# Kernel optimization log

Measured on AMD Instinct MI355X. Metric: run time of the kernel, lower is better.

Reference implementation:

```python
import jax, jax.numpy as jnp
import numpy as np

NUM_HEADS = 4
HEAD_K = 256
HEAD_V = 512
CHUNK = 64
GATE_NORMALIZER = 16.0
EPS = 1e-5


def _gla_chunk(q, k, v, gk):
    """Chunked gated linear attention.
    q,k,gk: [B,H,S,Dk]; v: [B,H,S,Dv]. gk is log-decay (<=0).
    Recurrence: S_t = diag(exp(gk_t)) S_{t-1} + k_t v_t^T ; o_t = scale * q_t S_t.
    """
    B, H, S, Dk = q.shape
    Dv = v.shape[-1]
    N = S // CHUNK
    scale = Dk ** -0.5

    def to_chunks(x):
        # [B,H,S,D] -> [N,B,H,C,D]
        return x.reshape(B, H, N, CHUNK, x.shape[-1]).transpose(2, 0, 1, 3, 4)

    qc, kc, vc, gkc = map(to_chunks, (q, k, v, gk))
    gc = jnp.cumsum(gkc, axis=-2)  # inclusive cumulative log-decay within chunk

    tri = jnp.tril(jnp.ones((CHUNK, CHUNK), dtype=q.dtype))  # causal incl. diagonal

    def step(Sstate, xs):
        qi, ki, vi, gi = xs  # [B,H,C,Dk]/[B,H,C,Dv]
        q_g = qi * jnp.exp(gi) * scale            # [B,H,C,Dk]
        k_g = ki * jnp.exp(-gi)                   # [B,H,C,Dk]
        A = jnp.einsum('bhid,bhjd->bhij', q_g, k_g) * tri
        o_intra = jnp.einsum('bhij,bhjе->bhiе'.replace('е', 'e'), A, vi)
        o_inter = jnp.einsum('bhcd,bhde->bhce', q_g, Sstate)
        g_last = gi[:, :, -1, :]                  # [B,H,Dk]
        k_dec = ki * jnp.exp(g_last[:, :, None, :] - gi)
        S_new = Sstate * jnp.exp(g_last)[..., None] + jnp.einsum('bhcd,bhce->bhde', k_dec, vi)
        return S_new, o_intra + o_inter

    S0 = jnp.zeros((B, H, Dk, Dv), dtype=q.dtype)
    _, o = jax.lax.scan(step, S0, (qc, kc, vc, gc))
    # [N,B,H,C,Dv] -> [B,H,S,Dv]
    return o.transpose(1, 2, 0, 3, 4).reshape(B, H, S, Dv)


def setup_inputs() -> dict:
    key = jax.random.key(0)
    ks = jax.random.split(key, 10)
    B, S, Hd = 2, 2048, 2048
    key_dim = NUM_HEADS * HEAD_K   # 1024
    value_dim = NUM_HEADS * HEAD_V  # 2048
    lr = 16  # gate_low_rank_dim
    w = lambda k, shp: (jax.random.normal(k, shp, dtype=jnp.float32) * 0.02)
    return {
        'hidden_states': jax.random.normal(ks[0], (B, S, Hd), dtype=jnp.float32),
        'Wq': w(ks[1], (Hd, key_dim)),
        'Wk': w(ks[2], (Hd, key_dim)),
        'Wv': w(ks[3], (Hd, value_dim)),
        'Wgk1': w(ks[4], (Hd, lr)),
        'Wgk2': w(ks[5], (lr, key_dim)),
        'bgk2': jnp.zeros((key_dim,), dtype=jnp.float32),
        'Wg': w(ks[6], (Hd, value_dim)),
        'g_norm_weight': jnp.ones((HEAD_V,), dtype=jnp.float32),
        'Wo': w(ks[7], (value_dim, Hd)),
    }


def reference(hidden_states, Wq, Wk, Wv, Wgk1, Wgk2, bgk2, Wg, g_norm_weight, Wo):
    B, S, Hd = hidden_states.shape
    x = hidden_states
    # projections
    q = (x @ Wq).reshape(B, S, NUM_HEADS, HEAD_K).transpose(0, 2, 1, 3)
    k = (x @ Wk).reshape(B, S, NUM_HEADS, HEAD_K).transpose(0, 2, 1, 3)
    v = (x @ Wv).reshape(B, S, NUM_HEADS, HEAD_V).transpose(0, 2, 1, 3)
    gk = (x @ Wgk1) @ Wgk2 + bgk2
    gk = jax.nn.log_sigmoid(gk) / GATE_NORMALIZER
    gk = gk.reshape(B, S, NUM_HEADS, HEAD_K).transpose(0, 2, 1, 3)

    o = _gla_chunk(q, k, v, gk)  # [B,H,S,Dv]
    o = o.transpose(0, 2, 1, 3)  # [B,S,H,Dv]

    # fused RMSNorm + swish gate
    g = (x @ Wg).reshape(B, S, NUM_HEADS, HEAD_V)
    rms = jnp.sqrt(jnp.mean(o * o, axis=-1, keepdims=True) + EPS)
    o = (o / rms) * g_norm_weight * (g * jax.nn.sigmoid(g))
    o = o.reshape(B, S, NUM_HEADS * HEAD_V)
    return o @ Wo
```

## Files before the change

### kernel.cpp

```cpp
#include <hip/hip_runtime.h>
#include <hip/hip_bf16.h>

#define B_   2
#define S_   2048
#define HD_  2048
#define H_   4
#define DK_  256
#define DV_  512
#define KD_  1024
#define VD_  2048
#define ND_  6144
#define M_   4096
#define NCHUNK_ 32
#define CHUNK_  64

typedef __attribute__((ext_vector_type(8))) short bf16x8;
typedef __attribute__((ext_vector_type(4))) float f32x4;
typedef __attribute__((ext_vector_type(4))) unsigned short us4;
typedef __attribute__((ext_vector_type(8))) unsigned short us8;

__device__ __forceinline__ unsigned short f2bf(float f) {
    __hip_bfloat16 h = __float2bfloat16(f);
    return *reinterpret_cast<unsigned short*>(&h);
}
__device__ __forceinline__ float bf2f(unsigned short u) {
    unsigned int x = ((unsigned int)u) << 16;
    return *reinterpret_cast<float*>(&x);
}

__global__ __launch_bounds__(256) void tr_w_all(const float* __restrict__ Wq,
                                                const float* __restrict__ Wk,
                                                const float* __restrict__ Wv,
                                                const float* __restrict__ Wg,
                                                const float* __restrict__ Wo,
                                                unsigned short* __restrict__ WcatT,
                                                unsigned short* __restrict__ WotT) {
    __shared__ float Ws[32][33];
    const int t = threadIdx.x;
    const int bx = blockIdx.x;
    const float* W; unsigned short* Wt; int N, nt;
    if (bx < 32)       { W = Wq; Wt = WcatT;                        N = 1024; nt = bx; }
    else if (bx < 64)  { W = Wk; Wt = WcatT + 1024 * 2048;          N = 1024; nt = bx - 32; }
    else if (bx < 128) { W = Wv; Wt = WcatT + 2048 * 2048;          N = 2048; nt = bx - 64; }
    else if (bx < 192) { W = Wg; Wt = WcatT + (size_t)4096 * 2048;  N = 2048; nt = bx - 128; }
    else               { W = Wo; Wt = WotT;                         N = 2048; nt = bx - 192; }
    const int n0 = nt * 32, k0 = blockIdx.y * 32;
    const int r = t >> 3, c4 = (t & 7) * 4;
    float4 a = *(const float4*)&W[(size_t)(k0 + r) * N + n0 + c4];
    Ws[r][c4 + 0] = a.x; Ws[r][c4 + 1] = a.y; Ws[r][c4 + 2] = a.z; Ws[r][c4 + 3] = a.w;
    __syncthreads();
    const int nr = t >> 3, kc4 = (t & 7) * 4;
    us4 w;
#pragma unroll
    for (int j = 0; j < 4; ++j) w[j] = f2bf(Ws[kc4 + j][nr]);
    *(us4*)&Wt[(size_t)(n0 + nr) * 2048 + k0 + kc4] = w;
}

__global__ __launch_bounds__(256) void tr_v(const unsigned short* __restrict__ qkvg,
                                            unsigned short* __restrict__ vT) {
    __shared__ unsigned short Ws[32][36];
    const int t = threadIdx.x;
    const int c0 = blockIdx.x * 32;
    const int s0 = blockIdx.y * 32;
    {
        const int r = t >> 3, c4 = (t & 7) * 4;
        us4 w = *(const us4*)&qkvg[(size_t)(s0 + r) * ND_ + 2048 + c0 + c4];
        *(us4*)&Ws[r][c4] = w;
    }
    __syncthreads();
    const int er = t >> 3, sc4 = (t & 7) * 4;
    const int c = c0 + er;
    const int h = c >> 9, e = c & 511;
    const int b = s0 >> 11, srow = s0 & 2047;
    us4 w;
#pragma unroll
    for (int j = 0; j < 4; ++j) w[j] = Ws[sc4 + j][er];
    *(us4*)&vT[((size_t)(b * H_ + h) * 512 + e) * 2048 + srow + sc4] = w;
}

__global__ __launch_bounds__(256) void gemm_bt(const unsigned short* __restrict__ A,
                                               const unsigned short* __restrict__ Bt,
                                               float* __restrict__ Cf,
                                               unsigned short* __restrict__ Cb,
                                               int M, int N, int K) {
    __shared__ __align__(16) unsigned short As[128 * 64];
    __shared__ __align__(16) unsigned short Bs[128 * 64];
    const int t = threadIdx.x;
    const int m0 = blockIdx.y * 128, n0 = blockIdx.x * 128;
    const int wave = t >> 6, lane = t & 63;
    const int quad = lane >> 4, l16 = lane & 15;
    const int wm = (wave >> 1) * 64, wn = (wave & 1) * 64;

    f32x4 acc[4][4] = {};

    int aoff[4], boff[4], soff[4];
#pragma unroll
    for (int p = 0; p < 4; ++p) {
        int q = t + p * 256;
        int row = q >> 3, c = (q & 7) * 8;
        soff[p] = row * 64 + (c ^ ((row & 7) * 8));
        aoff[p] = (m0 + row) * K + c;
        boff[p] = (n0 + row) * K + c;
    }

    us8 pa[4], pb[4];
#pragma unroll
    for (int p = 0; p < 4; ++p) {
        pa[p] = *(const us8*)&A[aoff[p]];
        pb[p] = *(const us8*)&Bt[boff[p]];
    }

    for (int k0 = 0; k0 < K; k0 += 64) {
        __syncthreads();
#pragma unroll
        for (int p = 0; p < 4; ++p) {
            *(us8*)&As[soff[p]] = pa[p];
            *(us8*)&Bs[soff[p]] = pb[p];
        }
        __syncthreads();
        if (k0 + 64 < K) {
#pragma unroll
            for (int p = 0; p < 4; ++p) {
                pa[p] = *(const us8*)&A[aoff[p] + k0 + 64];
                pb[p] = *(const us8*)&Bt[boff[p] + k0 + 64];
            }
        }

#pragma unroll
        for (int ks = 0; ks < 2; ++ks) {
            bf16x8 af[4], bfr[4];
#pragma unroll
            for (int i = 0; i < 4; ++i) {
                int r = wm + i * 16 + l16;
                af[i] = *(const bf16x8*)&As[r * 64 + ((ks * 32 + quad * 8) ^ ((r & 7) * 8))];
            }
#pragma unroll
            for (int j = 0; j < 4; ++j) {
                int r = wn + j * 16 + l16;
                bfr[j] = *(const bf16x8*)&Bs[r * 64 + ((ks * 32 + quad * 8) ^ ((r & 7) * 8))];
            }
#pragma unroll
            for (int i = 0; i < 4; ++i)
#pragma unroll
                for (int j = 0; j < 4; ++j)
                    acc[i][j] = __builtin_amdgcn_mfma_f32_16x16x32_bf16(af[i], bfr[j], acc[i][j], 0, 0, 0);
        }
    }

    if (Cb) {
#pragma unroll
        for (int i = 0; i < 4; ++i)
#pragma unroll
            for (int j = 0; j < 4; ++j)
#pragma unroll
                for (int r = 0; r < 4; ++r)
                    Cb[(size_t)(m0 + wm + i * 16 + quad * 4 + r) * N + n0 + wn + j * 16 + l16] = f2bf(acc[i][j][r]);
    } else {
#pragma unroll
        for (int i = 0; i < 4; ++i)
#pragma unroll
            for (int j = 0; j < 4; ++j)
#pragma unroll
                for (int r = 0; r < 4; ++r)
                    Cf[(size_t)(m0 + wm + i * 16 + quad * 4 + r) * N + n0 + wn + j * 16 + l16] = acc[i][j][r];
    }
}

__global__ __launch_bounds__(256) void gemm_n16(const float* __restrict__ X,
                                                const float* __restrict__ W,
                                                float* __restrict__ T,
                                                unsigned short* __restrict__ xb) {
    __shared__ float Xs[16][129];
    __shared__ float Wsh[128][17];
    const int t = threadIdx.x;
    const int m0 = blockIdx.x * 16;
    const int mm = t >> 4, jj = t & 15;
    float acc = 0.f;
    for (int k0 = 0; k0 < HD_; k0 += 128) {
        __syncthreads();
#pragma unroll
        for (int p = 0; p < 2; ++p) {
            int q = t + p * 256;
            int r = q >> 5, c4 = (q & 31) * 4;
            float4 a = *(const float4*)&X[(size_t)(m0 + r) * HD_ + k0 + c4];
            Xs[r][c4 + 0] = a.x; Xs[r][c4 + 1] = a.y; Xs[r][c4 + 2] = a.z; Xs[r][c4 + 3] = a.w;
            us4 wv; wv.x = f2bf(a.x); wv.y = f2bf(a.y); wv.z = f2bf(a.z); wv.w = f2bf(a.w);
            *(us4*)&xb[(size_t)(m0 + r) * HD_ + k0 + c4] = wv;
        }
#pragma unroll
        for (int p = 0; p < 8; ++p) {
            int q = t + p * 256;
            int r = q >> 4, c = q & 15;
            Wsh[r][c] = W[(size_t)(k0 + r) * 16 + c];
        }
        __syncthreads();
#pragma unroll 16
        for (int kk = 0; kk < 128; ++kk) acc += Xs[mm][kk] * Wsh[kk][jj];
    }
    T[(size_t)(m0 + mm) * 16 + jj] = acc;
}

__global__ __launch_bounds__(256) void gk_act(const float* __restrict__ T,
                                              const float* __restrict__ W2,
                                              const float* __restrict__ b2,
                                              float* __restrict__ gk) {
    const int idx = blockIdx.x * 256 + threadIdx.x;
    const int n = idx & 1023;
    const int m = idx >> 10;
    float acc = b2[n];
#pragma unroll
    for (int j = 0; j < 16; ++j) acc += T[m * 16 + j] * W2[j * 1024 + n];
    float ls = (acc < 0.f) ? (acc - log1pf(expf(acc))) : (-log1pf(expf(-acc)));
    gk[idx] = ls * 0.0625f;
}

__global__ __launch_bounds__(1024) void gate_prep(const unsigned short* __restrict__ qkvg,
                                                  const float* __restrict__ gk,
                                                  unsigned short* __restrict__ qg,
                                                  unsigned short* __restrict__ kg,
                                                  unsigned short* __restrict__ kgT,
                                                  float* __restrict__ glexp) {
    __shared__ unsigned short kgs[64][265];
    __shared__ float psum[4][256];
    const int tid = threadIdx.x;
    const int d = tid & 255;
    const int ts = tid >> 8;
    const int bhc = blockIdx.x;
    const int chunk = bhc & 31, bh = bhc >> 5;
    const int h = bh & 3, b = bh >> 2;
    const int col = h * 256 + d;
    const size_t row0 = (size_t)b * S_ + chunk * 64 + ts * 16;

    float g16[16];
    float part = 0.f;
#pragma unroll
    for (int i = 0; i < 16; ++i) {
        g16[i] = gk[(row0 + i) * (size_t)KD_ + col];
        part += g16[i];
    }
    psum[ts][d] = part;
    __syncthreads();
    float gc = 0.f;
#pragma unroll
    for (int j = 0; j < 3; ++j) if (j < ts) gc += psum[j][d];

    const float scale = 0.0625f;
#pragma unroll
    for (int i = 0; i < 16; ++i) {
        gc += g16[i];
        size_t r = row0 + i;
        unsigned short qv = qkvg[r * (size_t)ND_ + col];
        unsigned short kv = qkvg[r * (size_t)ND_ + 1024 + col];
        unsigned short kgv = f2bf(bf2f(kv) * expf(-gc));
        qg[r * (size_t)KD_ + col] = f2bf(bf2f(qv) * expf(gc) * scale);
        kg[r * (size_t)KD_ + col] = kgv;
        kgs[ts * 16 + i][d] = kgv;
    }
    if (ts == 3) glexp[((size_t)bh * 32 + chunk) * 256 + d] = expf(gc);
    __syncthreads();

    const size_t kgTbase = ((size_t)bh * 256) * 2048 + chunk * 64;
#pragma unroll
    for (int p = 0; p < 2; ++p) {
        int q = p * 1024 + tid;
        int dd = q >> 3, t8 = (q & 7) * 8;
        us8 w;
#pragma unroll
        for (int i = 0; i < 8; ++i) w[i] = kgs[t8 + i][dd];
        *(us8*)&kgT[kgTbase + (size_t)dd * 2048 + t8] = w;
    }
}

__global__ __launch_bounds__(256) void pass_c1(const unsigned short* __restrict__ qg,
                                               const unsigned short* __restrict__ kg,
                                               unsigned short* __restrict__ Asg) {
    __shared__ __align__(16) unsigned short Aq[64 * 40];
    __shared__ __align__(16) unsigned short Bk[64 * 40];
    const int t = threadIdx.x;
    const int bhc = blockIdx.x;
    const int chunk = bhc & 31, bh = bhc >> 5;
    const int h = bh & 3, b = bh >> 2;
    const int s0 = chunk * 64;
    const int wave = t >> 6, lane = t & 63;
    const int quad = lane >> 4, l16 = lane & 15;
    const int srow = t >> 2, scol = (t & 3) * 8;
    const size_t base = (size_t)b * S_ * KD_ + h * DK_ + (size_t)(s0 + srow) * KD_ + scol;

    f32x4 acc[4] = {};
    us8 aq = *(const us8*)&qg[base];
    us8 bk = *(const us8*)&kg[base];

    for (int k0 = 0; k0 < 256; k0 += 32) {
        __syncthreads();
        *(us8*)&Aq[srow * 40 + scol] = aq;
        *(us8*)&Bk[srow * 40 + scol] = bk;
        __syncthreads();
        if (k0 + 32 < 256) {
            aq = *(const us8*)&qg[base + k0 + 32];
            bk = *(const us8*)&kg[base + k0 + 32];
        }
        bf16x8 bfr = *(const bf16x8*)&Bk[(wave * 16 + l16) * 40 + quad * 8];
#pragma unroll
        for (int i = 0; i < 4; ++i) {
            bf16x8 af = *(const bf16x8*)&Aq[(i * 16 + l16) * 40 + quad * 8];
            acc[i] = __builtin_amdgcn_mfma_f32_16x16x32_bf16(af, bfr, acc[i], 0, 0, 0);
        }
    }

    const int j = wave * 16 + l16;
#pragma unroll
    for (int i = 0; i < 4; ++i)
#pragma unroll
        for (int r = 0; r < 4; ++r) {
            int m = i * 16 + quad * 4 + r;
            float val = (j <= m) ? acc[i][r] : 0.f;
            Asg[(size_t)bhc * 4096 + m * 64 + j] = f2bf(val);
        }
}

__global__ __launch_bounds__(256) void pass_ab(const unsigned short* __restrict__ kgT,
                                               const unsigned short* __restrict__ vT,
                                               const float* __restrict__ gle,
                                               unsigned short* __restrict__ St) {
    __shared__ __align__(16) unsigned short As[32 * 72];
    __shared__ __align__(16) unsigned short Bs[64 * 72];
    const int t = threadIdx.x;
    const int d0 = blockIdx.x * 64;
    const int e0 = blockIdx.y * 32;
    const int bh = blockIdx.z;
    const int wave = t >> 6, lane = t & 63;
    const int quad = lane >> 4, l16 = lane & 15;
    const int wm = (wave >> 1) * 16;
    const int wn = (wave & 1) * 32;
    const int srow = t >> 3, sc8 = (t & 7) * 8;

    const size_t vb  = ((size_t)bh * 512 + e0 + srow) * 2048 + sc8;
    const size_t kb0 = ((size_t)bh * 256 + d0 + srow) * 2048 + sc8;
    const size_t kb1 = ((size_t)bh * 256 + d0 + 32 + srow) * 2048 + sc8;

    f32x4 S[2] = {};

    for (int n = 0; n < NCHUNK_; ++n) {
        __syncthreads();
        *(us8*)&As[srow * 72 + sc8]        = *(const us8*)&vT[vb + n * 64];
        *(us8*)&Bs[srow * 72 + sc8]        = *(const us8*)&kgT[kb0 + n * 64];
        *(us8*)&Bs[(srow + 32) * 72 + sc8] = *(const us8*)&kgT[kb1 + n * 64];
        __syncthreads();

        f32x4 acc[2] = {};
#pragma unroll
        for (int ks = 0; ks < 2; ++ks) {
            bf16x8 af = *(const bf16x8*)&As[(wm + l16) * 72 + ks * 32 + quad * 8];
#pragma unroll
            for (int j = 0; j < 2; ++j) {
                bf16x8 bfr = *(const bf16x8*)&Bs[(wn + j * 16 + l16) * 72 + ks * 32 + quad * 8];
                acc[j] = __builtin_amdgcn_mfma_f32_16x16x32_bf16(af, bfr, acc[j], 0, 0, 0);
            }
        }

        const float E0 = gle[((size_t)bh * 32 + n) * 256 + d0 + wn + l16];
        const float E1 = gle[((size_t)bh * 32 + n) * 256 + d0 + wn + 16 + l16];
        const size_t obase = ((size_t)(bh * 32 + n)) * 512;
#pragma unroll
        for (int j = 0; j < 2; ++j) {
            const float E = j ? E1 : E0;
#pragma unroll
            for (int r = 0; r < 4; ++r) {
                size_t e = e0 + wm + quad * 4 + r;
                size_t d = d0 + wn + j * 16 + l16;
                St[(obase + e) * 256 + d] = f2bf(S[j][r]);
                S[j][r] = (S[j][r] + acc[j][r]) * E;
            }
        }
    }
}

__global__ __launch_bounds__(256) void pass_c2(const unsigned short* __restrict__ qg,
                                               const unsigned short* __restrict__ vT,
                                               const unsigned short* __restrict__ Asg,
                                               const unsigned short* __restrict__ St,
                                               unsigned short* __restrict__ o) {
    __shared__ __align__(16) unsigned short At[64 * 40];
    __shared__ __align__(16) unsigned short Bt[256 * 40];
    const int t = threadIdx.x;
    const int bhc = blockIdx.z;
    const int chunk = bhc & 31, bh = bhc >> 5;
    const int h = bh & 3, b = bh >> 2;
    const int s0 = chunk * 64;
    const int eh = blockIdx.x * 256;
    const int wave = t >> 6, lane = t & 63;
    const int quad = lane >> 4, l16 = lane & 15;
    const int we = wave * 64;

    f32x4 acc[4][4] = {};

    for (int kk0 = 0; kk0 < 10; ++kk0) {
        __syncthreads();
        if (kk0 < 2) {
            {
                int row = t >> 2, c8 = (t & 3) * 8;
                us8 w = *(const us8*)&Asg[(size_t)bhc * 4096 + row * 64 + kk0 * 32 + c8];
                *(us8*)&At[row * 40 + c8] = w;
            }
            const int t0 = kk0 * 32;
#pragma unroll
            for (int p = 0; p < 4; ++p) {
                int q = t + p * 256;
                int row = q >> 2, c8 = (q & 3) * 8;
                us8 w = *(const us8*)&vT[((size_t)bh * 512 + eh + row) * 2048 + s0 + t0 + c8];
                *(us8*)&Bt[row * 40 + c8] = w;
            }
        } else {
            const int d0 = (kk0 - 2) * 32;
            {
                int row = t >> 2, c8 = (t & 3) * 8;
                us8 w = *(const us8*)&qg[((size_t)b * S_ + s0 + row) * KD_ + h * DK_ + d0 + c8];
                *(us8*)&At[row * 40 + c8] = w;
            }
#pragma unroll
            for (int p = 0; p < 4; ++p) {
                int q = t + p * 256;
                int row = q >> 2, c8 = (q & 3) * 8;
                us8 w = *(const us8*)&St[(((size_t)bhc) * 512 + eh + row) * 256 + d0 + c8];
                *(us8*)&Bt[row * 40 + c8] = w;
            }
        }
        __syncthreads();

        bf16x8 af[4], bfr[4];
#pragma unroll
        for (int i = 0; i < 4; ++i)
            af[i] = *(const bf16x8*)&At[(i * 16 + l16) * 40 + quad * 8];
#pragma unroll
        for (int j = 0; j < 4; ++j)
            bfr[j] = *(const bf16x8*)&Bt[(we + j * 16 + l16) * 40 + quad * 8];
#pragma unroll
        for (int i = 0; i < 4; ++i)
#pragma unroll
            for (int j = 0; j < 4; ++j)
                acc[i][j] = __builtin_amdgcn_mfma_f32_16x16x32_bf16(af[i], bfr[j], acc[i][j], 0, 0, 0);
    }

#pragma unroll
    for (int i = 0; i < 4; ++i)
#pragma unroll
        for (int j = 0; j < 4; ++j)
#pragma unroll
            for (int r = 0; r < 4; ++r) {
                int m = i * 16 + quad * 4 + r;
                int e = eh + we + j * 16 + l16;
                o[((size_t)b * S_ + s0 + m) * VD_ + h * DV_ + e] = f2bf(acc[i][j][r]);
            }
}

__global__ __launch_bounds__(256) void postnorm(const unsigned short* __restrict__ o,
                                                const unsigned short* __restrict__ qkvg,
                                                const float* __restrict__ gnw,
                                                unsigned short* __restrict__ obf) {
    const int row = blockIdx.x;
    const int wave = threadIdx.x >> 6;
    const int lane = threadIdx.x & 63;
    const size_t base = (size_t)row * VD_ + wave * 512;
    const size_t gbase = (size_t)row * ND_ + 4096 + wave * 512;
    float x[8];
    float ss = 0.f;
#pragma unroll
    for (int j = 0; j < 8; ++j) {
        x[j] = bf2f(o[base + lane + j * 64]);
        ss += x[j] * x[j];
    }
#pragma unroll
    for (int off = 32; off; off >>= 1) ss += __shfl_xor(ss, off);
    const float inv = 1.0f / sqrtf(ss * (1.0f / 512.0f) + 1e-5f);
#pragma unroll
    for (int j = 0; j < 8; ++j) {
        int e = lane + j * 64;
        float gv = bf2f(qkvg[gbase + e]);
        float sig = 1.0f / (1.0f + expf(-gv));
        obf[base + e] = f2bf(x[j] * inv * gnw[e] * (gv * sig));
    }
}

extern "C" void kernel_launch(void* const* d_in, const int* in_sizes, int n_in,
                              void* d_out, int out_size, void* d_ws, size_t ws_size,
                              hipStream_t stream) {
    const float* x    = (const float*)d_in[0];
    const float* Wq   = (const float*)d_in[1];
    const float* Wk   = (const float*)d_in[2];
    const float* Wv   = (const float*)d_in[3];
    const float* Wgk1 = (const float*)d_in[4];
    const float* Wgk2 = (const float*)d_in[5];
    const float* bgk2 = (const float*)d_in[6];
    const float* Wg   = (const float*)d_in[7];
    const float* gnw  = (const float*)d_in[8];
    const float* Wo   = (const float*)d_in[9];
    float* out = (float*)d_out;

    float* ws = (float*)d_ws;
    const size_t MF = 1048576;
    typedef unsigned short us;
    us* WotT   = (us*)(ws);
    us* qkvg   = (us*)(ws + 2 * MF);
    us* qg     = (us*)(ws + 15 * MF);
    us* kg     = (us*)(ws + 17 * MF);
    us* kgT    = (us*)(ws + 19 * MF);
    us* vT     = (us*)(ws + 21 * MF);
    float* T   = ws + 25 * MF;
    float* gle = T + 65536;
    us* Asg    = (us*)(ws + 25 * MF + 131072);
    us* DtSt   = (us*)(ws + 25 * MF + 786432);
    us* xb     = (us*)(ws + 41 * MF + 786432);
    float* gkb = ws + 41 * MF + 786432;
    us* WcatT  = (us*)(ws + 45 * MF + 786432);
    us* o      = (us*)(ws + 45 * MF + 786432);
    us* obf    = (us*)(ws + 49 * MF + 786432);

    dim3 blk(256);
    gemm_n16<<<M_ / 16, blk, 0, stream>>>(x, Wgk1, T, xb);
    tr_w_all<<<dim3(256, 64), blk, 0, stream>>>(Wq, Wk, Wv, Wg, Wo, WcatT, WotT);

    gemm_bt<<<dim3(48, 32), blk, 0, stream>>>(xb, WcatT, nullptr, qkvg, M_, ND_, HD_);
    tr_v<<<dim3(64, 128), blk, 0, stream>>>(qkvg, vT);

    gk_act<<<(M_ * KD_) / 256, blk, 0, stream>>>(T, Wgk2, bgk2, gkb);
    gate_prep<<<256, dim3(1024), 0, stream>>>(qkvg, gkb, qg, kg, kgT, gle);

    pass_c1<<<256, blk, 0, stream>>>(qg, kg, Asg);
    pass_ab<<<dim3(4, 16, 8), blk, 0, stream>>>(kgT, vT, gle, DtSt);
    pass_c2<<<dim3(2, 1, 256), blk, 0, stream>>>(qg, vT, Asg, DtSt, o);
    postnorm<<<M_, blk, 0, stream>>>(o, qkvg, gnw, obf);
    gemm_bt<<<dim3(16, 32), blk, 0, stream>>>(obf, WotT, out, nullptr, M_, HD_, VD_);
}
```

Measured before the change: 439.0 us.

## Prefetch next tiles into registers in gk gemm, state scan and output kernels

Adds register double-buffering to three kernels (gemm_n16, the chunk state scan, pass_c2). Global loads for the next iteration are issued right after the shared-memory barrier, so they overlap with the MFMA or FMA compute of the current tile instead of stalling before it. This costs extra registers per thread, which could reduce occupancy.

```diff
diff --git a/kernel.cpp b/kernel.cpp
--- a/kernel.cpp
+++ b/kernel.cpp
@@ -175,25 +175,51 @@
     const int t = threadIdx.x;
     const int m0 = blockIdx.x * 16;
     const int mm = t >> 4, jj = t & 15;
+
+    int xr[2], xc[2];
+#pragma unroll
+    for (int p = 0; p < 2; ++p) {
+        int q = t + p * 256;
+        xr[p] = q >> 5; xc[p] = (q & 31) * 4;
+    }
+    float4 px[2];
+    float pw[8];
+#pragma unroll
+    for (int p = 0; p < 2; ++p)
+        px[p] = *(const float4*)&X[(size_t)(m0 + xr[p]) * HD_ + xc[p]];
+#pragma unroll
+    for (int p = 0; p < 8; ++p) {
+        int q = t + p * 256;
+        pw[p] = W[(size_t)(q >> 4) * 16 + (q & 15)];
+    }
+
     float acc = 0.f;
     for (int k0 = 0; k0 < HD_; k0 += 128) {
         __syncthreads();
 #pragma unroll
         for (int p = 0; p < 2; ++p) {
-            int q = t + p * 256;
-            int r = q >> 5, c4 = (q & 31) * 4;
-            float4 a = *(const float4*)&X[(size_t)(m0 + r) * HD_ + k0 + c4];
-            Xs[r][c4 + 0] = a.x; Xs[r][c4 + 1] = a.y; Xs[r][c4 + 2] = a.z; Xs[r][c4 + 3] = a.w;
+            float4 a = px[p];
+            Xs[xr[p]][xc[p] + 0] = a.x; Xs[xr[p]][xc[p] + 1] = a.y;
+            Xs[xr[p]][xc[p] + 2] = a.z; Xs[xr[p]][xc[p] + 3] = a.w;
             us4 wv; wv.x = f2bf(a.x); wv.y = f2bf(a.y); wv.z = f2bf(a.z); wv.w = f2bf(a.w);
-            *(us4*)&xb[(size_t)(m0 + r) * HD_ + k0 + c4] = wv;
+            *(us4*)&xb[(size_t)(m0 + xr[p]) * HD_ + k0 + xc[p]] = wv;
         }
 #pragma unroll
         for (int p = 0; p < 8; ++p) {
             int q = t + p * 256;
-            int r = q >> 4, c = q & 15;
-            Wsh[r][c] = W[(size_t)(k0 + r) * 16 + c];
-        }
-        __syncthreads();
+            Wsh[q >> 4][q & 15] = pw[p];
+        }
+        __syncthreads();
+        if (k0 + 128 < HD_) {
+#pragma unroll
+            for (int p = 0; p < 2; ++p)
+                px[p] = *(const float4*)&X[(size_t)(m0 + xr[p]) * HD_ + k0 + 128 + xc[p]];
+#pragma unroll
+            for (int p = 0; p < 8; ++p) {
+                int q = t + p * 256;
+                pw[p] = W[(size_t)(k0 + 128 + (q >> 4)) * 16 + (q & 15)];
+            }
+        }
 #pragma unroll 16
         for (int kk = 0; kk < 128; ++kk) acc += Xs[mm][kk] * Wsh[kk][jj];
     }
@@ -337,15 +363,30 @@
     const size_t vb  = ((size_t)bh * 512 + e0 + srow) * 2048 + sc8;
     const size_t kb0 = ((size_t)bh * 256 + d0 + srow) * 2048 + sc8;
     const size_t kb1 = ((size_t)bh * 256 + d0 + 32 + srow) * 2048 + sc8;
+    const size_t gbase = (size_t)bh * 32 * 256 + d0 + wn + l16;
 
     f32x4 S[2] = {};
 
+    us8 pv  = *(const us8*)&vT[vb];
+    us8 pk0 = *(const us8*)&kgT[kb0];
+    us8 pk1 = *(const us8*)&kgT[kb1];
+    float pE0 = gle[gbase];
+    float pE1 = gle[gbase + 16];
+
     for (int n = 0; n < NCHUNK_; ++n) {
         __syncthreads();
-        *(us8*)&As[srow * 72 + sc8]        = *(const us8*)&vT[vb + n * 64];
-        *(us8*)&Bs[srow * 72 + sc8]        = *(const us8*)&kgT[kb0 + n * 64];
-        *(us8*)&Bs[(srow + 32) * 72 + sc8] = *(const us8*)&kgT[kb1 + n * 64];
-        __syncthreads();
+        *(us8*)&As[srow * 72 + sc8]        = pv;
+        *(us8*)&Bs[srow * 72 + sc8]        = pk0;
+        *(us8*)&Bs[(srow + 32) * 72 + sc8] = pk1;
+        __syncthreads();
+        const float E0 = pE0, E1 = pE1;
+        if (n + 1 < NCHUNK_) {
+            pv  = *(const us8*)&vT[vb + (n + 1) * 64];
+            pk0 = *(const us8*)&kgT[kb0 + (n + 1) * 64];
+            pk1 = *(const us8*)&kgT[kb1 + (n + 1) * 64];
+            pE0 = gle[gbase + (n + 1) * 256];
+            pE1 = gle[gbase + (n + 1) * 256 + 16];
+        }
 
         f32x4 acc[2] = {};
 #pragma unroll
@@ -358,8 +399,6 @@
             }
         }
 
-        const float E0 = gle[((size_t)bh * 32 + n) * 256 + d0 + wn + l16];
-        const float E1 = gle[((size_t)bh * 32 + n) * 256 + d0 + wn + 16 + l16];
         const size_t obase = ((size_t)(bh * 32 + n)) * 512;
 #pragma unroll
         for (int j = 0; j < 2; ++j) {
@@ -391,41 +430,51 @@
     const int wave = t >> 6, lane = t & 63;
     const int quad = lane >> 4, l16 = lane & 15;
     const int we = wave * 64;
+    const int arow = t >> 2, ac8 = (t & 3) * 8;
 
     f32x4 acc[4][4] = {};
+    us8 pa, pb[4];
+
+    pa = *(const us8*)&Asg[(size_t)bhc * 4096 + arow * 64 + ac8];
+#pragma unroll
+    for (int p = 0; p < 4; ++p) {
+        int q = t + p * 256;
+        int row = q >> 2, c8 = (q & 3) * 8;
+        pb[p] = *(const us8*)&vT[((size_t)bh * 512 + eh + row) * 2048 + s0 + c8];
+    }
 
     for (int kk0 = 0; kk0 < 10; ++kk0) {
         __syncthreads();
-        if (kk0 < 2) {
-            {
-                int row = t >> 2, c8 = (t & 3) * 8;
-                us8 w = *(const us8*)&Asg[(size_t)bhc * 4096 + row * 64 + kk0 * 32 + c8];
-                *(us8*)&At[row * 40 + c8] = w;
-            }
-            const int t0 = kk0 * 32;
-#pragma unroll
-            for (int p = 0; p < 4; ++p) {
-                int q = t + p * 256;
-                int row = q >> 2, c8 = (q & 3) * 8;
-                us8 w = *(const us8*)&vT[((size_t)bh * 512 + eh + row) * 2048 + s0 + t0 + c8];
-                *(us8*)&Bt[row * 40 + c8] = w;
-            }
-        } else {
-            const int d0 = (kk0 - 2) * 32;
-            {
-                int row = t >> 2, c8 = (t & 3) * 8;
-                us8 w = *(const us8*)&qg[((size_t)b * S_ + s0 + row) * KD_ + h * DK_ + d0 + c8];
-                *(us8*)&At[row * 40 + c8] = w;
-            }
-#pragma unroll
-            for (int p = 0; p < 4; ++p) {
-                int q = t + p * 256;
-                int row = q >> 2, c8 = (q & 3) * 8;
-                us8 w = *(const us8*)&St[(((size_t)bhc) * 512 + eh + row) * 256 + d0 + c8];
-                *(us8*)&Bt[row * 40 + c8] = w;
-            }
-        }
-        __syncthreads();
+        *(us8*)&At[arow * 40 + ac8] = pa;
+#pragma unroll
+        for (int p = 0; p < 4; ++p) {
+            int q = t + p * 256;
+            int row = q >> 2, c8 = (q & 3) * 8;
+            *(us8*)&Bt[row * 40 + c8] = pb[p];
+        }
+        __syncthreads();
+
+        if (kk0 + 1 < 10) {
+            const int nx = kk0 + 1;
+            if (nx < 2) {
+                pa = *(const us8*)&Asg[(size_t)bhc * 4096 + arow * 64 + nx * 32 + ac8];
+#pragma unroll
+                for (int p = 0; p < 4; ++p) {
+                    int q = t + p * 256;
+                    int row = q >> 2, c8 = (q & 3) * 8;
+                    pb[p] = *(const us8*)&vT[((size_t)bh * 512 + eh + row) * 2048 + s0 + nx * 32 + c8];
+                }
+            } else {
+                const int d0 = (nx - 2) * 32;
+                pa = *(const us8*)&qg[((size_t)b * S_ + s0 + arow) * KD_ + h * DK_ + d0 + ac8];
+#pragma unroll
+                for (int p = 0; p < 4; ++p) {
+                    int q = t + p * 256;
+                    int row = q >> 2, c8 = (q & 3) * 8;
+                    pb[p] = *(const us8*)&St[(((size_t)bhc) * 512 + eh + row) * 256 + d0 + c8];
+                }
+            }
+        }
 
         bf16x8 af[4], bfr[4];
 #pragma unroll
```

Result: slower. 460.9 us (+5.0%).
